# Performance work log

Hardware: AMD Instinct MI355X
Metric: run time of the kernel (lower is better)

## Reference

```python
import jax, jax.numpy as jnp
import numpy as np
import math

B, N, C = 1, 2048, 256
H, CH = 8, 32
PQ, PV = 8, 12
CZ = 32
BQ, BK = 32, 128
NB = N // BQ
PAD = (BK - BQ) // 2
INF = 1e8
EPS = 1e-8

_KIDX = np.arange(NB)[:, None] * BQ + np.arange(BK)[None, :] - PAD
_KVALID = (_KIDX >= 0) & (_KIDX < N)
_KIDX_C = np.clip(_KIDX, 0, N - 1)


def _quat_to_rot(q):
    q = q / jnp.linalg.norm(q, axis=-1, keepdims=True)
    w, x, y, z = q[..., 0], q[..., 1], q[..., 2], q[..., 3]
    return jnp.stack([
        jnp.stack([1 - 2 * (y * y + z * z), 2 * (x * y - w * z), 2 * (x * z + w * y)], -1),
        jnp.stack([2 * (x * y + w * z), 1 - 2 * (x * x + z * z), 2 * (y * z - w * x)], -1),
        jnp.stack([2 * (x * z - w * y), 2 * (y * z + w * x), 1 - 2 * (x * x + y * y)], -1)], -2)


def _to_queries(x):
    # [B, N, ...] -> [B, NB, BQ, ...]
    return x.reshape((B, NB, BQ) + x.shape[2:])


def _to_keys(x):
    # [B, N, ...] -> [B, NB, BK, ...] zero-padded sliding key windows
    g = x[:, _KIDX_C]
    v = jnp.asarray(_KVALID, x.dtype).reshape((1, NB, BK) + (1,) * (x.ndim - 2))
    return g * v


def _ln(x):
    m = x.mean(-1, keepdims=True)
    var = x.var(-1, keepdims=True)
    return (x - m) / jnp.sqrt(var + 1e-5)


def setup_inputs():
    key = jax.random.key(0)
    ks = jax.random.split(key, 16)
    p = 0.02
    return {
        's': jax.random.normal(ks[0], (B, N, C), jnp.float32),
        'cond': jax.random.normal(ks[1], (B, N, C), jnp.float32),
        'z': jax.random.normal(ks[2], (B, NB, BQ, BK, CZ), jnp.float32),
        'trans': jax.random.normal(ks[3], (B, N, 3), jnp.float32),
        'rots': _quat_to_rot(jax.random.normal(ks[4], (B, N, 4), jnp.float32)),
        's_mask': jnp.ones((B, N), jnp.float32),
        'Wq': jax.random.normal(ks[5], (C, H * CH)) * p,
        'Wk': jax.random.normal(ks[6], (C, H * CH)) * p,
        'Wv': jax.random.normal(ks[7], (C, H * CH)) * p,
        'Wqp': jax.random.normal(ks[8], (C, H * PQ * 3)) * p,
        'Wkvp': jax.random.normal(ks[9], (C, H * (PQ + PV) * 3)) * p,
        'Wb': jax.random.normal(ks[10], (CZ, H)) * p,
        'Wdz': jax.random.normal(ks[11], (CZ, CZ // 4)) * p,
        'head_weights': jnp.full((H,), 0.5413),
        'Wout': jax.random.normal(ks[12], (H * (CZ // 4 + CH + PV * 4), C)) * p,
        'Wg': jax.random.normal(ks[13], (C, C)) * p,
        'bg': jnp.zeros((C,)),
        'Wbeta': jax.random.normal(ks[14], (C, C)) * p,
        'bbeta': jnp.zeros((C,)),
        'g_z': jnp.ones((CZ,)),
        'b_z': jnp.zeros((CZ,)),
    }


def reference(s, cond, z, trans, rots, s_mask, Wq, Wk, Wv, Wqp, Wkvp, Wb, Wdz,
              head_weights, Wout, Wg, bg, Wbeta, bbeta, g_z, b_z):
    # AdaLN on s conditioned on cond; LayerNorm on z
    s = _ln(s) * (cond @ Wg + bg) + (cond @ Wbeta + bbeta)
    z = _ln(z) * g_z + b_z

    q_in = _to_queries(s)            # [B,NB,BQ,C]
    k_in = _to_keys(s)               # [B,NB,BK,C]
    q_t = _to_queries(trans)         # [B,NB,BQ,3]
    q_R = _to_queries(rots)          # [B,NB,BQ,3,3]
    k_t = _to_keys(trans)
    k_R = _to_keys(rots)
    # zero-padded key rotations -> identity
    zero = jnp.all(k_R == 0, axis=(-2, -1))[..., None, None]
    k_R = jnp.where(zero, jnp.eye(3, dtype=k_R.dtype), k_R)

    q = (q_in @ Wq).reshape(B, NB, BQ, H, CH)
    k = (k_in @ Wk).reshape(B, NB, BK, H, CH)
    v = (k_in @ Wv).reshape(B, NB, BK, H, CH)

    q_pts = (q_in @ Wqp).reshape(B, NB, BQ, H * PQ, 3)
    q_pts = jnp.einsum('bnqij,bnqpj->bnqpi', q_R, q_pts) + q_t[..., None, :]
    q_pts = q_pts.reshape(B, NB, BQ, H, PQ, 3)

    kv_pts = (k_in @ Wkvp).reshape(B, NB, BK, H * (PQ + PV), 3)
    kv_pts = jnp.einsum('bnkij,bnkpj->bnkpi', k_R, kv_pts) + k_t[..., None, :]
    kv_pts = kv_pts.reshape(B, NB, BK, H, PQ + PV, 3)
    k_pts, v_pts = kv_pts[..., :PQ, :], kv_pts[..., PQ:, :]

    b = z @ Wb                                    # [B,NB,BQ,BK,H]
    a = jnp.einsum('bnqhc,bnkhc->bnqkh', q, k) * math.sqrt(1.0 / (3 * CH))
    a = a + math.sqrt(1.0 / 3.0) * b

    disp = q_pts[:, :, :, None] - k_pts[:, :, None]   # [B,NB,BQ,BK,H,PQ,3]
    d2 = jnp.sum(disp * disp, axis=-1)                # [B,NB,BQ,BK,H,PQ]
    hw = jax.nn.softplus(head_weights) * math.sqrt(1.0 / (3 * (PQ * 9.0 / 2)))
    pt_att = -0.5 * jnp.sum(d2 * hw[:, None], axis=-1)   # [B,NB,BQ,BK,H]

    m_q = _to_queries(s_mask[..., None])              # [B,NB,BQ,1]
    m_k = _to_keys(s_mask[..., None])                 # [B,NB,BK,1]
    attn_mask = m_q * jnp.swapaxes(m_k, -1, -2)       # [B,NB,BQ,BK]
    attn_mask = INF * (attn_mask - 1.0)

    a = a + pt_att + attn_mask[..., None]
    a = jnp.swapaxes(a, -1, -2)                       # [B,NB,BQ,H,BK]
    a = jax.nn.softmax(a, axis=-1)

    o = jnp.einsum('bnqhk,bnkhc->bnqhc', a, v).reshape(B, NB, BQ, H * CH)
    o_pt = jnp.einsum('bnqhk,bnkhvc->bnqhvc', a, v_pts)      # [B,NB,BQ,H,PV,3]
    o_pt = jnp.einsum('bnqji,bnqhvj->bnqhvi', q_R,
                      o_pt - q_t[:, :, :, None, None, :])     # invert apply
    o_pt_norm = jnp.sqrt(jnp.sum(o_pt ** 2, -1) + EPS).reshape(B, NB, BQ, H * PV)
    o_pt = o_pt.reshape(B, NB, BQ, H * PV * 3)
    pair_z = z @ Wdz                                          # [B,NB,BQ,BK,CZ//4]
    o_pair = jnp.einsum('bnqhk,bnqkc->bnqhc', a, pair_z).reshape(B, NB, BQ, H * (CZ // 4))

    out = jnp.concatenate([o, o_pt, o_pt_norm, o_pair], -1) @ Wout
    return out.reshape(B, N, C)
```

## Files before the change

### kernel.cpp

```cpp
#include <hip/hip_runtime.h>
#include <hip/hip_bf16.h>
#include <math.h>

typedef __hip_bfloat16 bf16;
typedef __attribute__((ext_vector_type(8))) short short8;
typedef __attribute__((ext_vector_type(4))) short short4v;
typedef __attribute__((ext_vector_type(4))) float f32x4;

#define NRES 2048
#define CDIM 256
#define PADK 48
#define POS 1440

static __device__ __forceinline__ float b2f(bf16 x) { return __bfloat162float(x); }
static __device__ __forceinline__ float us2f(short u) {
    return __uint_as_float(((unsigned)(unsigned short)u) << 16);
}
static __device__ __forceinline__ short f2s(float f) {
    bf16 h = __float2bfloat16(f);
    return *reinterpret_cast<short*>(&h);
}
static __device__ __forceinline__ bool flag_f32(const void* smask) {
    return *(const unsigned int*)smask == 0x3F800000u;
}
static __device__ __forceinline__ float dual_load(const void* p, size_t i, bool f32) {
    float vf = ((const float*)p)[f32 ? i : 0];
    float vb = b2f(((const bf16*)p)[f32 ? (size_t)0 : i]);
    return f32 ? vf : vb;
}

struct PrepTable {
    const void* src[8];
    bf16* dst[8];
    int srcN[8];
    int nOff[8];
    int dstStride[8];
    float scl[8];
    int tileOff[9];
    const void* s;
    float* RS;
    const void* cond;
    bf16* condb;
    const void* rots;
    const void* trans;
    float* RT;
    const void* z;
    const void* Wb;
    const void* Wdz;
    const void* g_z;
    const void* b_z;
    bf16* Bzb;
    bf16* PZb;
};
__global__ __launch_bounds__(256) void k_prep(PrepTable tb, const void* __restrict__ smask) {
    __shared__ float tile[32][33];
    __shared__ float wb[32][8], wdz[32][8], gz[32], bz[32];
    bool f32 = flag_f32(smask);
    int b = blockIdx.x;
    int t = threadIdx.x;
    if (b < 1024) {
        {
            int j = t >> 3, c = t & 7;
            wb[j][c] = 0.5773502691896258f * dual_load(tb.Wb, t, f32);
            wdz[j][c] = dual_load(tb.Wdz, t, f32);
        }
        if (t < 32) { gz[t] = dual_load(tb.g_z, t, f32); bz[t] = dual_load(tb.b_z, t, f32); }
        __syncthreads();
        size_t r = (size_t)b * 256 + t;
        float zv[32];
        float sum = 0.f, sq = 0.f;
        if (f32) {
            const float4* zp = (const float4*)((const float*)tb.z + r * 32);
#pragma unroll
            for (int j4 = 0; j4 < 8; ++j4) {
                float4 v4 = zp[j4];
                zv[j4 * 4 + 0] = v4.x; zv[j4 * 4 + 1] = v4.y; zv[j4 * 4 + 2] = v4.z; zv[j4 * 4 + 3] = v4.w;
            }
        } else {
            const bf16* zp = (const bf16*)tb.z + r * 32;
#pragma unroll
            for (int j = 0; j < 32; ++j) zv[j] = b2f(zp[j]);
        }
#pragma unroll
        for (int j = 0; j < 32; ++j) { float v = zv[j]; sum += v; sq += v * v; }
        float m = sum / 32.f;
        float var = fmaxf(sq / 32.f - m * m, 0.f);
        float rstd = rsqrtf(var + 1e-5f);
#pragma unroll
        for (int j = 0; j < 32; ++j) zv[j] = (zv[j] - m) * rstd * gz[j] + bz[j];
        float bacc[8], pacc[8];
#pragma unroll
        for (int c = 0; c < 8; ++c) { bacc[c] = 0.f; pacc[c] = 0.f; }
        for (int j = 0; j < 32; ++j) {
            float v = zv[j];
#pragma unroll
            for (int c = 0; c < 8; ++c) { bacc[c] += v * wb[j][c]; pacc[c] += v * wdz[j][c]; }
        }
        int n = (int)(r >> 12);
        int q = (int)(r >> 7) & 31;
        int k = (int)r & 127;
#pragma unroll
        for (int h = 0; h < 8; ++h)
            tb.Bzb[(size_t)n * 32768 + (size_t)h * 4096 + q * 128 + k] = __float2bfloat16(bacc[h]);
#pragma unroll
        for (int c = 0; c < 8; ++c)
            tb.PZb[(((size_t)(n * 32 + q)) * 8 + c) * 128 + k] = __float2bfloat16(pacc[c]);
        return;
    }
    b -= 1024;
    if (b < tb.tileOff[8]) {
        int s = 0;
        while (b >= tb.tileOff[s + 1]) ++s;
        int rel = b - tb.tileOff[s];
        int ntTiles = tb.srcN[s] >> 5;
        int kt = rel / ntTiles, nt = rel % ntTiles;
        const void* src = tb.src[s];
        int srcN = tb.srcN[s];
        float scl = tb.scl[s];
        int tx = t & 31, ty = t >> 5;
#pragma unroll
        for (int r = 0; r < 4; ++r) {
            int srow = kt * 32 + ty + r * 8;
            int scol = nt * 32 + tx;
            tile[ty + r * 8][tx] = dual_load(src, (size_t)srow * srcN + scol, f32);
        }
        __syncthreads();
        bf16* dst = tb.dst[s];
#pragma unroll
        for (int r = 0; r < 4; ++r) {
            int n = nt * 32 + ty + r * 8 + tb.nOff[s];
            int k = kt * 32 + tx;
            dst[(size_t)n * tb.dstStride[s] + k] = __float2bfloat16(tile[tx][ty + r * 8] * scl);
        }
        return;
    }
    b -= tb.tileOff[8];
    if (b < 256) {
        int i0 = b * 2048;
        for (int i = t; i < 2048; i += 256)
            tb.condb[i0 + i] = __float2bfloat16(dual_load(tb.cond, (size_t)(i0 + i), f32));
        return;
    }
    b -= 256;
    if (b < 256) {
        int wave = t >> 6, lane = t & 63;
        int r0 = b * 8;
        for (int rr = 0; rr < 2; ++rr) {
            int row = r0 + wave * 2 + rr;
            float sum = 0.f, sq = 0.f;
            for (int j = lane; j < CDIM; j += 64) {
                float v = dual_load(tb.s, (size_t)row * CDIM + j, f32);
                sum += v; sq += v * v;
            }
            for (int off = 32; off; off >>= 1) { sum += __shfl_xor(sum, off); sq += __shfl_xor(sq, off); }
            if (lane == 0) {
                float m = sum / CDIM;
                float var = fmaxf(sq / CDIM - m * m, 0.f);
                tb.RS[row * 2 + 0] = m;
                tb.RS[row * 2 + 1] = rsqrtf(var + 1e-5f);
            }
        }
        return;
    }
    b -= 256;
    int i = b * 256 + t;
    int row = i / 12, c = i % 12;
    float v = (c < 9) ? dual_load(tb.rots, (size_t)row * 9 + c, f32)
                      : dual_load(tb.trans, (size_t)row * 3 + (c - 9), f32);
    tb.RT[i] = v;
}

__global__ __launch_bounds__(256) void k_gb(
    const bf16* __restrict__ condb, const bf16* __restrict__ GWt,
    const void* __restrict__ s, const float* __restrict__ RS,
    const void* __restrict__ bg, const void* __restrict__ bbeta,
    const void* __restrict__ smask, bf16* __restrict__ SQb)
{
    bool f32 = flag_f32(smask);
    int wid = threadIdx.x >> 6, lane = threadIdx.x & 63;
    int tid = blockIdx.x * 4 + wid;
    int mt = tid >> 4, nt = tid & 15;
    int idx = lane & 15, quad = lane >> 4;
    const bf16* Ap = condb + (size_t)(mt * 16 + idx) * 256 + quad * 8;
    const bf16* B0 = GWt + (size_t)(nt * 16 + idx) * 256 + quad * 8;
    const bf16* B1 = GWt + (size_t)(256 + nt * 16 + idx) * 256 + quad * 8;
    f32x4 a0 = {0,0,0,0}, a1 = {0,0,0,0};
#pragma unroll
    for (int k = 0; k < 256; k += 32) {
        short8 af = *(const short8*)(Ap + k);
        a0 = __builtin_amdgcn_mfma_f32_16x16x32_bf16(af, *(const short8*)(B0 + k), a0, 0, 0, 0);
        a1 = __builtin_amdgcn_mfma_f32_16x16x32_bf16(af, *(const short8*)(B1 + k), a1, 0, 0, 0);
    }
    int ocol = nt * 16 + idx;
    float bgc = dual_load(bg, ocol, f32), bbc = dual_load(bbeta, ocol, f32);
    int orow = mt * 16 + quad * 4;
#pragma unroll
    for (int r = 0; r < 4; ++r) {
        int row = orow + r;
        float sv = dual_load(s, (size_t)row * 256 + ocol, f32);
        float xn = (sv - RS[row * 2]) * RS[row * 2 + 1];
        SQb[(size_t)row * 256 + ocol] = __float2bfloat16(xn * (a0[r] + bgc) + (a1[r] + bbc));
    }
}

__global__ __launch_bounds__(256) void k_gemm22b(
    const bf16* __restrict__ A, const bf16* __restrict__ Bt, bf16* __restrict__ C,
    int N, int totalWaves)
{
    int wid = threadIdx.x >> 6, lane = threadIdx.x & 63;
    int tid = blockIdx.x * 4 + wid;
    if (tid >= totalWaves) return;
    int tiles_n = N >> 5;
    int mt = tid / tiles_n, nt = tid % tiles_n;
    int idx = lane & 15, quad = lane >> 4;
    const bf16* Ap0 = A + (size_t)(mt * 32 + idx) * 256 + quad * 8;
    const bf16* Ap1 = Ap0 + (size_t)16 * 256;
    const bf16* Bp0 = Bt + (size_t)(nt * 32 + idx) * 256 + quad * 8;
    const bf16* Bp1 = Bp0 + (size_t)16 * 256;
    f32x4 a00 = {0,0,0,0}, a01 = {0,0,0,0}, a10 = {0,0,0,0}, a11 = {0,0,0,0};
#pragma unroll 4
    for (int k = 0; k < 256; k += 32) {
        short8 af0 = *(const short8*)(Ap0 + k);
        short8 af1 = *(const short8*)(Ap1 + k);
        short8 bf0 = *(const short8*)(Bp0 + k);
        short8 bf1 = *(const short8*)(Bp1 + k);
        a00 = __builtin_amdgcn_mfma_f32_16x16x32_bf16(af0, bf0, a00, 0, 0, 0);
        a01 = __builtin_amdgcn_mfma_f32_16x16x32_bf16(af0, bf1, a01, 0, 0, 0);
        a10 = __builtin_amdgcn_mfma_f32_16x16x32_bf16(af1, bf0, a10, 0, 0, 0);
        a11 = __builtin_amdgcn_mfma_f32_16x16x32_bf16(af1, bf1, a11, 0, 0, 0);
    }
    int orow = mt * 32 + quad * 4;
    int ocol = nt * 32 + idx;
#pragma unroll
    for (int r = 0; r < 4; ++r) {
        C[(size_t)(orow + r) * N + ocol] = __float2bfloat16(a00[r]);
        C[(size_t)(orow + r) * N + ocol + 16] = __float2bfloat16(a01[r]);
        C[(size_t)(orow + r + 16) * N + ocol] = __float2bfloat16(a10[r]);
        C[(size_t)(orow + r + 16) * N + ocol + 16] = __float2bfloat16(a11[r]);
    }
}

__global__ __launch_bounds__(256, 4) void k_attn_out(
    const bf16* __restrict__ POb,
    const bf16* __restrict__ Bzb, const bf16* __restrict__ PZb,
    const float* __restrict__ RT,
    const void* __restrict__ smask, const void* __restrict__ head_weights,
    bf16* __restrict__ CATb)
{
    __shared__ char buf[39232];
    __shared__ float rowq[16], rowk[128], mk[128], mqv[16];
    short* VtS = (short*)buf;
    short* KpS = (short*)(buf + 21760);
    short* QpS = (short*)(buf + 29952);
    float* S   = (float*)(buf + 30976);
    short* AsS = (short*)(buf + 30976);
    float* OPT = (float*)(buf + 35328);

    const int bx = blockIdx.x;
    const int n = bx >> 4, h = (bx >> 1) & 7, qh = bx & 1;
    const int t = threadIdx.x;
    const bool f32 = flag_f32(smask);
    const int n32 = n * 32;
    const int q0 = qh * 16;
    const int rowg = n32 + q0;

    const int wid = t >> 6, lane = t & 63, idx = lane & 15, quad = lane >> 4;

    float hwv = dual_load(head_weights, h, f32);
    float ptc = -0.5f * log1pf(expf(hwv)) * 0.09622504486493764f;
    float m2ptc = -2.f * ptc;
    const short8 zero8 = {0,0,0,0,0,0,0,0};

    short8 afeat = *(const short8*)(POb + (size_t)(rowg + idx) * POS + h * 32 + quad * 8);
    short8 bfeat[2];
#pragma unroll
    for (int i = 0; i < 2; ++i) {
        int nt = wid * 2 + i;
        int kg = n32 + nt * 16 + idx - PADK;
        bfeat[i] = (kg >= 0 && kg < NRES)
            ? *(const short8*)(POb + (size_t)kg * POS + 256 + h * 32 + quad * 8) : zero8;
    }
    short bzr[8];
#pragma unroll
    for (int i = 0; i < 2; ++i) {
        int nt = wid * 2 + i;
        int k = nt * 16 + idx;
#pragma unroll
        for (int r = 0; r < 4; ++r) {
            int q = quad * 4 + r;
            bzr[i * 4 + r] = *(const short*)(Bzb + (size_t)n * 32768 + (size_t)h * 4096 + (q0 + q) * 128 + k);
        }
    }
    float4 kr0, kr1, kr2;
    float kmv = 0.f;
    short4v kpts[15];
    const int kgR = n32 + t - PADK;
    const bool validR = (t < 128) && (kgR >= 0 && kgR < NRES);
    if (validR) {
        const float4* rt = (const float4*)(RT + (size_t)kgR * 12);
        kr0 = rt[0]; kr1 = rt[1]; kr2 = rt[2];
        kmv = dual_load(smask, kgR, f32);
        const short4v* pp = (const short4v*)(POb + (size_t)kgR * POS + 960 + h * 60);
#pragma unroll
        for (int g = 0; g < 15; ++g) kpts[g] = pp[g];
    }
    float4 qr0, qr1, qr2;
    float qmv = 0.f;
    short8 qpts[3];
    if (t >= 240) {
        int q = t - 240;
        const float4* rt = (const float4*)(RT + (size_t)(rowg + q) * 12);
        qr0 = rt[0]; qr1 = rt[1]; qr2 = rt[2];
        qmv = dual_load(smask, rowg + q, f32);
        const short8* pp = (const short8*)(POb + (size_t)(rowg + q) * POS + 768 + h * 24);
#pragma unroll
        for (int g = 0; g < 3; ++g) qpts[g] = pp[g];
    }

    for (int i = t; i < 512; i += 256) {
        int k = i >> 2, g = i & 3;
        int kg = n32 + k - PADK;
        short8 v = zero8;
        if (kg >= 0 && kg < NRES)
            v = *(const short8*)(POb + (size_t)kg * POS + 512 + h * 32 + g * 8);
#pragma unroll
        for (int j = 0; j < 8; ++j) VtS[(g * 8 + j) * 136 + k] = v[j];
    }
    if (t < 128) {
        int k = t;
        if (validR) {
            const short* kp = (const short*)kpts;
            float s2 = 0.f;
#pragma unroll
            for (int j = 0; j < 20; ++j) {
                float x = us2f(kp[j * 3 + 0]);
                float y = us2f(kp[j * 3 + 1]);
                float z = us2f(kp[j * 3 + 2]);
                float p0 = kr0.x * x + kr0.y * y + kr0.z * z + kr2.y;
                float p1 = kr0.w * x + kr1.x * y + kr1.y * z + kr2.z;
                float p2 = kr1.z * x + kr1.w * y + kr2.x * z + kr2.w;
                if (j < 8) {
                    KpS[k * 32 + j * 3 + 0] = f2s(p0);
                    KpS[k * 32 + j * 3 + 1] = f2s(p1);
                    KpS[k * 32 + j * 3 + 2] = f2s(p2);
                    s2 += p0 * p0 + p1 * p1 + p2 * p2;
                } else {
                    int v = j - 8;
                    VtS[(32 + v * 3 + 0) * 136 + k] = f2s(p0);
                    VtS[(32 + v * 3 + 1) * 136 + k] = f2s(p1);
                    VtS[(32 + v * 3 + 2) * 136 + k] = f2s(p2);
                }
            }
            *(short8*)(KpS + k * 32 + 24) = zero8;
            rowk[k] = ptc * s2;
            mk[k] = kmv;
        } else {
#pragma unroll
            for (int g = 0; g < 4; ++g) *(short8*)(KpS + k * 32 + g * 8) = zero8;
            for (int x = 32; x < 68; ++x) VtS[x * 136 + k] = 0;
            rowk[k] = 0.f; mk[k] = 0.f;
        }
    } else if (t >= 240) {
        int q = t - 240;
        const short* qp = (const short*)qpts;
        float s2 = 0.f;
#pragma unroll
        for (int p = 0; p < 8; ++p) {
            float x = us2f(qp[p * 3 + 0]);
            float y = us2f(qp[p * 3 + 1]);
            float z = us2f(qp[p * 3 + 2]);
            float p0 = qr0.x * x + qr0.y * y + qr0.z * z + qr2.y;
            float p1 = qr0.w * x + qr1.x * y + qr1.y * z + qr2.z;
            float p2 = qr1.z * x + qr1.w * y + qr2.x * z + qr2.w;
            QpS[q * 32 + p * 3 + 0] = f2s(m2ptc * p0);
            QpS[q * 32 + p * 3 + 1] = f2s(m2ptc * p1);
            QpS[q * 32 + p * 3 + 2] = f2s(m2ptc * p2);
            s2 += p0 * p0 + p1 * p1 + p2 * p2;
        }
        *(short8*)(QpS + q * 32 + 24) = zero8;
        rowq[q] = ptc * s2;
        mqv[q] = qmv;
    }
    __syncthreads();

    short8 a2 = *(const short8*)(QpS + idx * 32 + quad * 8);
#pragma unroll
    for (int i = 0; i < 2; ++i) {
        int nt = wid * 2 + i;
        f32x4 acc = {0.f, 0.f, 0.f, 0.f};
        acc = __builtin_amdgcn_mfma_f32_16x16x32_bf16(afeat, bfeat[i], acc, 0, 0, 0);
        short8 b2 = *(const short8*)(KpS + (nt * 16 + idx) * 32 + quad * 8);
        acc = __builtin_amdgcn_mfma_f32_16x16x32_bf16(a2, b2, acc, 0, 0, 0);
        int k = nt * 16 + idx;
#pragma unroll
        for (int r = 0; r < 4; ++r) {
            int q = quad * 4 + r;
            float msk = 1e8f * (mqv[q] * mk[k] - 1.f);
            S[q * 129 + k] = acc[r] + us2f(bzr[i * 4 + r]) + rowq[q] + rowk[k] + msk;
        }
    }
    __syncthreads();

    float sa0[4], sa1[4];
#pragma unroll
    for (int rr = 0; rr < 4; ++rr) {
        int q = wid * 4 + rr;
        float v0 = S[q * 129 + lane], v1 = S[q * 129 + lane + 64];
        float mx = fmaxf(v0, v1);
        for (int off = 32; off; off >>= 1) mx = fmaxf(mx, __shfl_xor(mx, off));
        float e0 = expf(v0 - mx), e1 = expf(v1 - mx);
        float sm = e0 + e1;
        for (int off = 32; off; off >>= 1) sm += __shfl_xor(sm, off);
        float inv = 1.f / sm;
        sa0[rr] = e0 * inv; sa1[rr] = e1 * inv;
    }
    __syncthreads();
#pragma unroll
    for (int rr = 0; rr < 4; ++rr) {
        int q = wid * 4 + rr;
        AsS[q * 136 + lane] = f2s(sa0[rr]);
        AsS[q * 136 + lane + 64] = f2s(sa1[rr]);
    }
    __syncthreads();

    short8 pz0[8];
    if (t < 128) {
        int q = t >> 3, c = t & 7;
        const short8* pzp = (const short8*)(PZb + ((size_t)(rowg + q) * 8 + c) * 128);
#pragma unroll
        for (int k8 = 0; k8 < 8; ++k8) pz0[k8] = pzp[k8];
    }
#pragma unroll
    for (int i = 0; i < 2; ++i) {
        int tt = wid + i * 4;
        if (tt >= 5) break;
        int nt = tt;
        f32x4 acc = {0.f, 0.f, 0.f, 0.f};
#pragma unroll
        for (int kk = 0; kk < 4; ++kk) {
            short8 af  = *(const short8*)(AsS + idx * 136 + kk * 32 + quad * 8);
            short8 bfv = *(const short8*)(VtS + (nt * 16 + idx) * 136 + kk * 32 + quad * 8);
            acc = __builtin_amdgcn_mfma_f32_16x16x32_bf16(af, bfv, acc, 0, 0, 0);
        }
        int x = nt * 16 + idx;
#pragma unroll
        for (int r = 0; r < 4; ++r) {
            int q = quad * 4 + r;
            if (x < 32)
                CATb[(size_t)(rowg + q) * 704 + h * 32 + x] = __float2bfloat16(acc[r]);
            else if (x < 68)
                OPT[q * 37 + (x - 32)] = acc[r];
        }
    }
    if (t < 128) {
        int q = t >> 3, c = t & 7;
        const short8* pzp = (const short8*)(PZb + ((size_t)(rowg + q) * 8 + c) * 128);
        const short8* asp = (const short8*)(AsS + q * 136);
        float acc = 0.f;
#pragma unroll
        for (int k8 = 0; k8 < 8; ++k8) {
            short8 pv = pz0[k8];
            short8 av = asp[k8];
#pragma unroll
            for (int j = 0; j < 8; ++j) acc += us2f(av[j]) * us2f(pv[j]);
        }
#pragma unroll
        for (int k8 = 0; k8 < 8; ++k8) pz0[k8] = pzp[8 + k8];
#pragma unroll
        for (int k8 = 0; k8 < 8; ++k8) {
            short8 pv = pz0[k8];
            short8 av = asp[8 + k8];
#pragma unroll
            for (int j = 0; j < 8; ++j) acc += us2f(av[j]) * us2f(pv[j]);
        }
        CATb[(size_t)(rowg + q) * 704 + 640 + h * 8 + c] = __float2bfloat16(acc);
    }
    __syncthreads();

    if (t < 192) {
        int q = t / 12, v = t % 12;
        int g = rowg + q;
        const float4* rt = (const float4*)(RT + (size_t)g * 12);
        float4 r0 = rt[0], r1 = rt[1], r2 = rt[2];
        float x = OPT[q * 37 + v * 3 + 0] - r2.y;
        float y = OPT[q * 37 + v * 3 + 1] - r2.z;
        float z = OPT[q * 37 + v * 3 + 2] - r2.w;
        float o0 = r0.x * x + r0.w * y + r1.z * z;
        float o1 = r0.y * x + r1.x * y + r1.w * z;
        float o2 = r0.z * x + r1.y * y + r2.x * z;
        size_t cb = (size_t)g * 704;
        CATb[cb + 256 + (h * 12 + v) * 3 + 0] = __float2bfloat16(o0);
        CATb[cb + 256 + (h * 12 + v) * 3 + 1] = __float2bfloat16(o1);
        CATb[cb + 256 + (h * 12 + v) * 3 + 2] = __float2bfloat16(o2);
        CATb[cb + 544 + h * 12 + v] = __float2bfloat16(sqrtf(o0 * o0 + o1 * o1 + o2 * o2 + 1e-8f));
    }
}

__global__ __launch_bounds__(256) void k_gemm(
    const bf16* __restrict__ A, const bf16* __restrict__ Bt, void* __restrict__ Cv,
    const void* __restrict__ smask)
{
    int wid = threadIdx.x >> 6, lane = threadIdx.x & 63;
    int tid = blockIdx.x * 4 + wid;
    int mt = tid >> 4, nt = tid & 15;
    int idx = lane & 15, quad = lane >> 4;
    const bf16* Ap = A + (size_t)(mt * 16 + idx) * 704 + quad * 8;
    const bf16* Bp = Bt + (size_t)(nt * 16 + idx) * 704 + quad * 8;
    f32x4 acc = {0.f, 0.f, 0.f, 0.f};
#pragma unroll 4
    for (int k = 0; k < 704; k += 32) {
        short8 af = *(const short8*)(Ap + k);
        short8 bfv = *(const short8*)(Bp + k);
        acc = __builtin_amdgcn_mfma_f32_16x16x32_bf16(af, bfv, acc, 0, 0, 0);
    }
    int orow = mt * 16 + quad * 4;
    int ocol = nt * 16 + idx;
    if (flag_f32(smask)) {
        float* C = (float*)Cv;
#pragma unroll
        for (int r = 0; r < 4; ++r) C[(size_t)(orow + r) * 256 + ocol] = acc[r];
    } else {
        bf16* C = (bf16*)Cv;
#pragma unroll
        for (int r = 0; r < 4; ++r) C[(size_t)(orow + r) * 256 + ocol] = __float2bfloat16(acc[r]);
    }
}

extern "C" void kernel_launch(void* const* d_in, const int* in_sizes, int n_in,
                              void* d_out, int out_size, void* d_ws, size_t ws_size,
                              hipStream_t stream) {
    const void* s       = d_in[0];
    const void* cond    = d_in[1];
    const void* z       = d_in[2];
    const void* trans   = d_in[3];
    const void* rots    = d_in[4];
    const void* s_mask  = d_in[5];
    const void* Wq      = d_in[6];
    const void* Wk      = d_in[7];
    const void* Wv      = d_in[8];
    const void* Wqp     = d_in[9];
    const void* Wkvp    = d_in[10];
    const void* Wb      = d_in[11];
    const void* Wdz     = d_in[12];
    const void* hweights= d_in[13];
    const void* Wout    = d_in[14];
    const void* Wg      = d_in[15];
    const void* bg      = d_in[16];
    const void* Wbeta   = d_in[17];
    const void* bbeta   = d_in[18];
    const void* g_z     = d_in[19];
    const void* b_z     = d_in[20];

    float* ws = (float*)d_ws;
    bf16* POb   = (bf16*)(ws);
    bf16* Bzb   = (bf16*)(ws + 1474560);
    bf16* PZb   = (bf16*)(ws + 2523136);
    bf16* SQb   = (bf16*)(ws + 3571712);
    bf16* condb = (bf16*)(ws + 3833856);
    bf16* CATb  = (bf16*)(ws + 4358144);
    bf16* PWt   = (bf16*)(ws + 5079040);
    bf16* GWt   = (bf16*)(ws + 5263360);
    bf16* FWt   = (bf16*)(ws + 5328896);
    float* RT   = (float*)(ws + 5419008);
    float* RS   = (float*)(ws + 5443584);

    PrepTable tb;
    const float qkscale = 0.10206207261596575f;
    tb.src[0] = Wq;   tb.dst[0] = PWt; tb.srcN[0] = 256; tb.nOff[0] = 0;   tb.dstStride[0] = 256; tb.scl[0] = qkscale;
    tb.src[1] = Wk;   tb.dst[1] = PWt; tb.srcN[1] = 256; tb.nOff[1] = 256; tb.dstStride[1] = 256; tb.scl[1] = 1.f;
    tb.src[2] = Wv;   tb.dst[2] = PWt; tb.srcN[2] = 256; tb.nOff[2] = 512; tb.dstStride[2] = 256; tb.scl[2] = 1.f;
    tb.src[3] = Wqp;  tb.dst[3] = PWt; tb.srcN[3] = 192; tb.nOff[3] = 768; tb.dstStride[3] = 256; tb.scl[3] = 1.f;
    tb.src[4] = Wkvp; tb.dst[4] = PWt; tb.srcN[4] = 480; tb.nOff[4] = 960; tb.dstStride[4] = 256; tb.scl[4] = 1.f;
    tb.src[5] = Wg;   tb.dst[5] = GWt; tb.srcN[5] = 256; tb.nOff[5] = 0;   tb.dstStride[5] = 256; tb.scl[5] = 1.f;
    tb.src[6] = Wbeta;tb.dst[6] = GWt; tb.srcN[6] = 256; tb.nOff[6] = 256; tb.dstStride[6] = 256; tb.scl[6] = 1.f;
    tb.src[7] = Wout; tb.dst[7] = FWt; tb.srcN[7] = 256; tb.nOff[7] = 0;   tb.dstStride[7] = 704; tb.scl[7] = 1.f;
    int tc[8] = {64, 64, 64, 48, 120, 64, 64, 176};
    tb.tileOff[0] = 0;
    for (int i = 0; i < 8; ++i) tb.tileOff[i + 1] = tb.tileOff[i] + tc[i];
    tb.s = s; tb.RS = RS;
    tb.cond = cond; tb.condb = condb;
    tb.rots = rots; tb.trans = trans; tb.RT = RT;
    tb.z = z; tb.Wb = Wb; tb.Wdz = Wdz; tb.g_z = g_z; tb.b_z = b_z;
    tb.Bzb = Bzb; tb.PZb = PZb;

    dim3 blk(256);
    k_prep<<<dim3(2296), blk, 0, stream>>>(tb, s_mask);
    k_gb<<<dim3(512), blk, 0, stream>>>(condb, GWt, s, RS, bg, bbeta, s_mask, SQb);
    k_gemm22b<<<dim3(720), blk, 0, stream>>>(SQb, PWt, POb, 1440, 2880);
    k_attn_out<<<dim3(1024), blk, 0, stream>>>(POb, Bzb, PZb, RT, s_mask, hweights, CATb);
    k_gemm<<<dim3(512), blk, 0, stream>>>(CATb, FWt, d_out, s_mask);
}
```

Before: 168.5 us.

## Move z layernorm/projection and RT packing into the projection GEMM launch

The pair-feature layernorm and projection (Bzb/PZb) and the rotation/translation packing move out of the prep kernel into the projection GEMM kernel as extra block ranges. This shortens the prep kernel on the critical path before the gate GEMM, and the large z pass now runs in the same grid as the independent projection GEMM so the two can fill the GPU together. The cost is a heavier combined kernel whose blocks have uneven shapes, and the z work now begins later, after the gate GEMM finishes.

```diff
diff --git a/kernel.cpp b/kernel.cpp
--- a/kernel.cpp
+++ b/kernel.cpp
@@ -41,73 +41,12 @@
     float* RS;
     const void* cond;
     bf16* condb;
-    const void* rots;
-    const void* trans;
-    float* RT;
-    const void* z;
-    const void* Wb;
-    const void* Wdz;
-    const void* g_z;
-    const void* b_z;
-    bf16* Bzb;
-    bf16* PZb;
 };
 __global__ __launch_bounds__(256) void k_prep(PrepTable tb, const void* __restrict__ smask) {
     __shared__ float tile[32][33];
-    __shared__ float wb[32][8], wdz[32][8], gz[32], bz[32];
     bool f32 = flag_f32(smask);
     int b = blockIdx.x;
     int t = threadIdx.x;
-    if (b < 1024) {
-        {
-            int j = t >> 3, c = t & 7;
-            wb[j][c] = 0.5773502691896258f * dual_load(tb.Wb, t, f32);
-            wdz[j][c] = dual_load(tb.Wdz, t, f32);
-        }
-        if (t < 32) { gz[t] = dual_load(tb.g_z, t, f32); bz[t] = dual_load(tb.b_z, t, f32); }
-        __syncthreads();
-        size_t r = (size_t)b * 256 + t;
-        float zv[32];
-        float sum = 0.f, sq = 0.f;
-        if (f32) {
-            const float4* zp = (const float4*)((const float*)tb.z + r * 32);
-#pragma unroll
-            for (int j4 = 0; j4 < 8; ++j4) {
-                float4 v4 = zp[j4];
-                zv[j4 * 4 + 0] = v4.x; zv[j4 * 4 + 1] = v4.y; zv[j4 * 4 + 2] = v4.z; zv[j4 * 4 + 3] = v4.w;
-            }
-        } else {
-            const bf16* zp = (const bf16*)tb.z + r * 32;
-#pragma unroll
-            for (int j = 0; j < 32; ++j) zv[j] = b2f(zp[j]);
-        }
-#pragma unroll
-        for (int j = 0; j < 32; ++j) { float v = zv[j]; sum += v; sq += v * v; }
-        float m = sum / 32.f;
-        float var = fmaxf(sq / 32.f - m * m, 0.f);
-        float rstd = rsqrtf(var + 1e-5f);
-#pragma unroll
-        for (int j = 0; j < 32; ++j) zv[j] = (zv[j] - m) * rstd * gz[j] + bz[j];
-        float bacc[8], pacc[8];
-#pragma unroll
-        for (int c = 0; c < 8; ++c) { bacc[c] = 0.f; pacc[c] = 0.f; }
-        for (int j = 0; j < 32; ++j) {
-            float v = zv[j];
-#pragma unroll
-            for (int c = 0; c < 8; ++c) { bacc[c] += v * wb[j][c]; pacc[c] += v * wdz[j][c]; }
-        }
-        int n = (int)(r >> 12);
-        int q = (int)(r >> 7) & 31;
-        int k = (int)r & 127;
-#pragma unroll
-        for (int h = 0; h < 8; ++h)
-            tb.Bzb[(size_t)n * 32768 + (size_t)h * 4096 + q * 128 + k] = __float2bfloat16(bacc[h]);
-#pragma unroll
-        for (int c = 0; c < 8; ++c)
-            tb.PZb[(((size_t)(n * 32 + q)) * 8 + c) * 128 + k] = __float2bfloat16(pacc[c]);
-        return;
-    }
-    b -= 1024;
     if (b < tb.tileOff[8]) {
         int s = 0;
         while (b >= tb.tileOff[s + 1]) ++s;
@@ -142,7 +81,7 @@
         return;
     }
     b -= 256;
-    if (b < 256) {
+    {
         int wave = t >> 6, lane = t & 63;
         int r0 = b * 8;
         for (int rr = 0; rr < 2; ++rr) {
@@ -160,14 +99,7 @@
                 tb.RS[row * 2 + 1] = rsqrtf(var + 1e-5f);
             }
         }
-        return;
-    }
-    b -= 256;
-    int i = b * 256 + t;
-    int row = i / 12, c = i % 12;
-    float v = (c < 9) ? dual_load(tb.rots, (size_t)row * 9 + c, f32)
-                      : dual_load(tb.trans, (size_t)row * 3 + (c - 9), f32);
-    tb.RT[i] = v;
+    }
 }
 
 __global__ __launch_bounds__(256) void k_gb(
@@ -203,41 +135,114 @@
     }
 }
 
-__global__ __launch_bounds__(256) void k_gemm22b(
-    const bf16* __restrict__ A, const bf16* __restrict__ Bt, bf16* __restrict__ C,
-    int N, int totalWaves)
-{
-    int wid = threadIdx.x >> 6, lane = threadIdx.x & 63;
-    int tid = blockIdx.x * 4 + wid;
-    if (tid >= totalWaves) return;
-    int tiles_n = N >> 5;
-    int mt = tid / tiles_n, nt = tid % tiles_n;
+struct GzArgs {
+    const bf16* SQb;
+    const bf16* PWt;
+    bf16* POb;
+    const void* z;
+    const void* Wb;
+    const void* Wdz;
+    const void* g_z;
+    const void* b_z;
+    bf16* Bzb;
+    bf16* PZb;
+    const void* rots;
+    const void* trans;
+    float* RT;
+};
+__global__ __launch_bounds__(256) void k_gemm_z(GzArgs a, const void* __restrict__ smask) {
+    __shared__ float wb[32][8], wdz[32][8], gz[32], bz[32];
+    bool f32 = flag_f32(smask);
+    int b = blockIdx.x;
+    int t = threadIdx.x;
+    int wid = t >> 6, lane = t & 63;
     int idx = lane & 15, quad = lane >> 4;
-    const bf16* Ap0 = A + (size_t)(mt * 32 + idx) * 256 + quad * 8;
-    const bf16* Ap1 = Ap0 + (size_t)16 * 256;
-    const bf16* Bp0 = Bt + (size_t)(nt * 32 + idx) * 256 + quad * 8;
-    const bf16* Bp1 = Bp0 + (size_t)16 * 256;
-    f32x4 a00 = {0,0,0,0}, a01 = {0,0,0,0}, a10 = {0,0,0,0}, a11 = {0,0,0,0};
+    if (b < 720) {
+        int tid = b * 4 + wid;
+        int mt = tid / 45, nt = tid % 45;
+        const bf16* Ap0 = a.SQb + (size_t)(mt * 32 + idx) * 256 + quad * 8;
+        const bf16* Ap1 = Ap0 + (size_t)16 * 256;
+        const bf16* Bp0 = a.PWt + (size_t)(nt * 32 + idx) * 256 + quad * 8;
+        const bf16* Bp1 = Bp0 + (size_t)16 * 256;
+        f32x4 a00 = {0,0,0,0}, a01 = {0,0,0,0}, a10 = {0,0,0,0}, a11 = {0,0,0,0};
 #pragma unroll 4
-    for (int k = 0; k < 256; k += 32) {
-        short8 af0 = *(const short8*)(Ap0 + k);
-        short8 af1 = *(const short8*)(Ap1 + k);
-        short8 bf0 = *(const short8*)(Bp0 + k);
-        short8 bf1 = *(const short8*)(Bp1 + k);
-        a00 = __builtin_amdgcn_mfma_f32_16x16x32_bf16(af0, bf0, a00, 0, 0, 0);
-        a01 = __builtin_amdgcn_mfma_f32_16x16x32_bf16(af0, bf1, a01, 0, 0, 0);
-        a10 = __builtin_amdgcn_mfma_f32_16x16x32_bf16(af1, bf0, a10, 0, 0, 0);
-        a11 = __builtin_amdgcn_mfma_f32_16x16x32_bf16(af1, bf1, a11, 0, 0, 0);
-    }
-    int orow = mt * 32 + quad * 4;
-    int ocol = nt * 32 + idx;
-#pragma unroll
-    for (int r = 0; r < 4; ++r) {
-        C[(size_t)(orow + r) * N + ocol] = __float2bfloat16(a00[r]);
-        C[(size_t)(orow + r) * N + ocol + 16] = __float2bfloat16(a01[r]);
-        C[(size_t)(orow + r + 16) * N + ocol] = __float2bfloat16(a10[r]);
-        C[(size_t)(orow + r + 16) * N + ocol + 16] = __float2bfloat16(a11[r]);
-    }
+        for (int k = 0; k < 256; k += 32) {
+            short8 af0 = *(const short8*)(Ap0 + k);
+            short8 af1 = *(const short8*)(Ap1 + k);
+            short8 bf0 = *(const short8*)(Bp0 + k);
+            short8 bf1 = *(const short8*)(Bp1 + k);
+            a00 = __builtin_amdgcn_mfma_f32_16x16x32_bf16(af0, bf0, a00, 0, 0, 0);
+            a01 = __builtin_amdgcn_mfma_f32_16x16x32_bf16(af0, bf1, a01, 0, 0, 0);
+            a10 = __builtin_amdgcn_mfma_f32_16x16x32_bf16(af1, bf0, a10, 0, 0, 0);
+            a11 = __builtin_amdgcn_mfma_f32_16x16x32_bf16(af1, bf1, a11, 0, 0, 0);
+        }
+        int orow = mt * 32 + quad * 4;
+        int ocol = nt * 32 + idx;
+#pragma unroll
+        for (int r = 0; r < 4; ++r) {
+            a.POb[(size_t)(orow + r) * POS + ocol] = __float2bfloat16(a00[r]);
+            a.POb[(size_t)(orow + r) * POS + ocol + 16] = __float2bfloat16(a01[r]);
+            a.POb[(size_t)(orow + r + 16) * POS + ocol] = __float2bfloat16(a10[r]);
+            a.POb[(size_t)(orow + r + 16) * POS + ocol + 16] = __float2bfloat16(a11[r]);
+        }
+        return;
+    }
+    b -= 720;
+    if (b < 1024) {
+        {
+            int j = t >> 3, c = t & 7;
+            wb[j][c] = 0.5773502691896258f * dual_load(a.Wb, t, f32);
+            wdz[j][c] = dual_load(a.Wdz, t, f32);
+        }
+        if (t < 32) { gz[t] = dual_load(a.g_z, t, f32); bz[t] = dual_load(a.b_z, t, f32); }
+        __syncthreads();
+        size_t r = (size_t)b * 256 + t;
+        float zv[32];
+        float sum = 0.f, sq = 0.f;
+        if (f32) {
+            const float4* zp = (const float4*)((const float*)a.z + r * 32);
+#pragma unroll
+            for (int j4 = 0; j4 < 8; ++j4) {
+                float4 v4 = zp[j4];
+                zv[j4 * 4 + 0] = v4.x; zv[j4 * 4 + 1] = v4.y; zv[j4 * 4 + 2] = v4.z; zv[j4 * 4 + 3] = v4.w;
+            }
+        } else {
+            const bf16* zp = (const bf16*)a.z + r * 32;
+#pragma unroll
+            for (int j = 0; j < 32; ++j) zv[j] = b2f(zp[j]);
+        }
+#pragma unroll
+        for (int j = 0; j < 32; ++j) { float v = zv[j]; sum += v; sq += v * v; }
+        float m = sum / 32.f;
+        float var = fmaxf(sq / 32.f - m * m, 0.f);
+        float rstd = rsqrtf(var + 1e-5f);
+#pragma unroll
+        for (int j = 0; j < 32; ++j) zv[j] = (zv[j] - m) * rstd * gz[j] + bz[j];
+        float bacc[8], pacc[8];
+#pragma unroll
+        for (int c = 0; c < 8; ++c) { bacc[c] = 0.f; pacc[c] = 0.f; }
+        for (int j = 0; j < 32; ++j) {
+            float v = zv[j];
+#pragma unroll
+            for (int c = 0; c < 8; ++c) { bacc[c] += v * wb[j][c]; pacc[c] += v * wdz[j][c]; }
+        }
+        int n = (int)(r >> 12);
+        int q = (int)(r >> 7) & 31;
+        int k = (int)r & 127;
+#pragma unroll
+        for (int h = 0; h < 8; ++h)
+            a.Bzb[(size_t)n * 32768 + (size_t)h * 4096 + q * 128 + k] = __float2bfloat16(bacc[h]);
+#pragma unroll
+        for (int c = 0; c < 8; ++c)
+            a.PZb[(((size_t)(n * 32 + q)) * 8 + c) * 128 + k] = __float2bfloat16(pacc[c]);
+        return;
+    }
+    b -= 1024;
+    int i = b * 256 + t;
+    int row = i / 12, c = i % 12;
+    float v = (c < 9) ? dual_load(a.rots, (size_t)row * 9 + c, f32)
+                      : dual_load(a.trans, (size_t)row * 3 + (c - 9), f32);
+    a.RT[i] = v;
 }
 
 __global__ __launch_bounds__(256, 4) void k_attn_out(
@@ -579,14 +584,17 @@
     for (int i = 0; i < 8; ++i) tb.tileOff[i + 1] = tb.tileOff[i] + tc[i];
     tb.s = s; tb.RS = RS;
     tb.cond = cond; tb.condb = condb;
-    tb.rots = rots; tb.trans = trans; tb.RT = RT;
-    tb.z = z; tb.Wb = Wb; tb.Wdz = Wdz; tb.g_z = g_z; tb.b_z = b_z;
-    tb.Bzb = Bzb; tb.PZb = PZb;
+
+    GzArgs ga;
+    ga.SQb = SQb; ga.PWt = PWt; ga.POb = POb;
+    ga.z = z; ga.Wb = Wb; ga.Wdz = Wdz; ga.g_z = g_z; ga.b_z = b_z;
+    ga.Bzb = Bzb; ga.PZb = PZb;
+    ga.rots = rots; ga.trans = trans; ga.RT = RT;
 
     dim3 blk(256);
-    k_prep<<<dim3(2296), blk, 0, stream>>>(tb, s_mask);
+    k_prep<<<dim3(1176), blk, 0, stream>>>(tb, s_mask);
     k_gb<<<dim3(512), blk, 0, stream>>>(condb, GWt, s, RS, bg, bbeta, s_mask, SQb);
-    k_gemm22b<<<dim3(720), blk, 0, stream>>>(SQb, PWt, POb, 1440, 2880);
+    k_gemm_z<<<dim3(1840), blk, 0, stream>>>(ga, s_mask);
     k_attn_out<<<dim3(1024), blk, 0, stream>>>(POb, Bzb, PZb, RT, s_mask, hweights, CATb);
     k_gemm<<<dim3(512), blk, 0, stream>>>(CATb, FWt, d_out, s_mask);
 }
```

After: 167.8 us. About the same (-0.4%).
